# Performance work log

Hardware: AMD Instinct MI355X
Metric: run time of the kernel (lower is better)

The kernel has to match this reference:

```python
import jax, jax.numpy as jnp
import numpy as np

N_NODES = 100000
N_EDGES = 1600000
IN_CH = 1024
FEAT_CH = 128
OUT_CH = 3


def setup_inputs() -> dict:
    key = jax.random.key(0)
    ks = jax.random.split(key, 9)
    features = jax.random.normal(ks[0], (N_NODES, IN_CH), dtype=jnp.float32)
    edges = jax.random.randint(ks[1], (2, N_EDGES), 0, N_NODES, dtype=jnp.int64)
    edges2 = jax.random.randint(ks[2], (2, N_EDGES), 0, N_NODES, dtype=jnp.int64)
    edge_features = jax.random.normal(ks[3], (N_EDGES, 1), dtype=jnp.float32)
    additional_feature = jax.random.normal(ks[4], (N_NODES, 20), dtype=jnp.float32)
    # GCNConv linear weights (glorot-ish scale) and biases
    W1 = jax.random.normal(ks[5], (IN_CH, FEAT_CH), dtype=jnp.float32) * (1.0 / np.sqrt(IN_CH))
    b1 = jnp.zeros((FEAT_CH,), dtype=jnp.float32)
    W2 = jax.random.normal(ks[6], (FEAT_CH, OUT_CH), dtype=jnp.float32) * (1.0 / np.sqrt(FEAT_CH))
    b2 = jnp.zeros((OUT_CH,), dtype=jnp.float32)
    return {"features": features, "edges": edges, "edges2": edges2,
            "edge_features": edge_features, "additional_feature": additional_feature,
            "W1": W1, "b1": b1, "W2": W2, "b2": b2}


def gcn_conv(x, edge_index, W, b, num_nodes):
    """PyG GCNConv: x' = D^{-1/2}(A+I)D^{-1/2} x W + b (self-loops added)."""
    x = x @ W  # project first (cheaper feature dim for aggregation)
    loop = jnp.arange(num_nodes, dtype=edge_index.dtype)
    src = jnp.concatenate([edge_index[0], loop])
    dst = jnp.concatenate([edge_index[1], loop])
    deg = jax.ops.segment_sum(jnp.ones_like(dst, dtype=x.dtype), dst,
                              num_segments=num_nodes)  # >=1 due to self-loops
    dinv = jax.lax.rsqrt(deg)
    norm = dinv[src] * dinv[dst]  # [E+N]
    out = jax.ops.segment_sum(x[src] * norm[:, None], dst, num_segments=num_nodes)
    return out + b


def reference(features, edges, edges2, edge_features, additional_feature, W1, b1, W2, b2):
    # use_additional_channels=False -> features unchanged; edge_features forced to None
    n = features.shape[0]
    x = gcn_conv(features, edges2, W1, b1, n)
    x = jax.nn.relu(x)
    # dropout inactive in eval mode
    return gcn_conv(x, edges2, W2, b2, n)
```

## Files before the change

kernel.cpp:

```cpp
#include <hip/hip_runtime.h>
#include <hip/hip_bf16.h>

typedef __attribute__((ext_vector_type(8))) _Float16 half8;
typedef __attribute__((ext_vector_type(4))) float f32x4;

#define N_NODES 100000
#define N_EDGES 1600000
#define IN_CH 1024
#define FEAT 128
#define CAP 64
#define NDIG 196
#define CAPC 10240
#define NGB ((N_NODES + 127) / 128)

__device__ __forceinline__ void gload16(const void* g, void* l) {
    __builtin_amdgcn_global_load_lds(
        (const __attribute__((address_space(1))) unsigned int*)g,
        (__attribute__((address_space(3))) unsigned int*)l, 16, 0, 0);
}

__global__ void k_prep(const float* __restrict__ W1, _Float16* __restrict__ Bf,
                       int* __restrict__ cursorC, int* __restrict__ done) {
    int idx = blockIdx.x * 256 + threadIdx.x;
    if (idx < IN_CH * FEAT) {
        int col = idx & (FEAT - 1), k = idx >> 7;
        int cf = col >> 4, s = k >> 5;
        int lane = ((k >> 3) & 3) * 16 + (col & 15);
        int e = k & 7;
        Bf[(((cf * 32 + s) * 64 + lane) << 3) + e] = (_Float16)W1[idx];
    }
    if (idx < NDIG) cursorC[idx] = idx * CAPC;
    if (idx == 0) *done = 0;
}

__global__ __launch_bounds__(256, 2) void k_build_gemm(
    const float* __restrict__ A, const _Float16* __restrict__ Bf,
    const int4* __restrict__ src4, const int4* __restrict__ dst4,
    int* __restrict__ cursorC, uint2* __restrict__ recs,
    int* __restrict__ csr, int* __restrict__ cnt, float* __restrict__ dinvarr,
    int* __restrict__ done, _Float16* __restrict__ H, int M, int e4)
{
    __shared__ union {
        float As[2][8192];
        struct { int hist[NDIG], segoff[NDIG], lcur[NDIG]; } bin;
        int cl[512];
    } sm;
    const int t = threadIdx.x;

    if (blockIdx.x < NDIG) {
        const int b = blockIdx.x;
        if (t < NDIG) sm.bin.hist[t] = 0;
        __syncthreads();
        const int base4 = b * 2048;
        int4 sv[8], dv[8];
#pragma unroll
        for (int j = 0; j < 8; ++j) {
            int idx = base4 + j * 256 + t;
            if (idx < e4) { sv[j] = src4[idx]; dv[j] = dst4[idx]; }
            else { sv[j] = (int4){-1,-1,-1,-1}; dv[j] = (int4){-1,-1,-1,-1}; }
        }
#pragma unroll
        for (int j = 0; j < 8; ++j) {
            int dd[4] = {dv[j].x, dv[j].y, dv[j].z, dv[j].w};
            int ss[4] = {sv[j].x, sv[j].y, sv[j].z, sv[j].w};
#pragma unroll
            for (int c = 0; c < 4; ++c)
                if ((unsigned)dd[c] < N_NODES && (unsigned)ss[c] < N_NODES)
                    atomicAdd(&sm.bin.hist[dd[c] >> 9], 1);
        }
        __syncthreads();
        if (t < NDIG) {
            sm.bin.segoff[t] = atomicAdd(&cursorC[t], sm.bin.hist[t]);
            sm.bin.lcur[t] = 0;
        }
        __syncthreads();
#pragma unroll
        for (int j = 0; j < 8; ++j) {
            int dd[4] = {dv[j].x, dv[j].y, dv[j].z, dv[j].w};
            int ss[4] = {sv[j].x, sv[j].y, sv[j].z, sv[j].w};
#pragma unroll
            for (int c = 0; c < 4; ++c) {
                if ((unsigned)dd[c] < N_NODES && (unsigned)ss[c] < N_NODES) {
                    int dg = dd[c] >> 9;
                    int r = atomicAdd(&sm.bin.lcur[dg], 1);
                    int pos = sm.bin.segoff[dg] + r;
                    if (pos < (dg + 1) * CAPC)
                        recs[pos] = (uint2){(unsigned)ss[c], (unsigned)dd[c]};
                }
            }
        }
        __syncthreads();
        if (t == 0) {
            __threadfence();
            __hip_atomic_fetch_add(done, 1, __ATOMIC_RELEASE, __HIP_MEMORY_SCOPE_AGENT);
            while (__hip_atomic_load(done, __ATOMIC_ACQUIRE, __HIP_MEMORY_SCOPE_AGENT) < NDIG)
                __builtin_amdgcn_s_sleep(8);
        }
        __syncthreads();
        const int d = blockIdx.x;
        for (int j = t; j < 512; j += 256) sm.cl[j] = 0;
        __syncthreads();
        const int base = d * CAPC;
        int n = cursorC[d] - base;
        if (n > CAPC) n = CAPC;
        for (int k = t; k < n; k += 256) {
            uint2 r = recs[base + k];
            int local = (int)r.y & 511;
            int slot = atomicAdd(&sm.cl[local], 1);
            if (slot < CAP) csr[((int)r.y << 6) + slot] = (int)r.x;
        }
        __syncthreads();
        const int node0 = d << 9;
        for (int j = t; j < 512; j += 256) {
            int node = node0 + j;
            if (node < N_NODES) {
                int c = sm.cl[j] < CAP ? sm.cl[j] : CAP;
                cnt[node] = c;
                dinvarr[node] = rsqrtf((float)(c + 1));
            }
        }
        return;
    }

    const int gb = blockIdx.x - NDIG;
    const int brow0 = gb << 7;
    const int wid = t >> 6, lane = t & 63;

    const char* gsrc[8];
#pragma unroll
    for (int i = 0; i < 8; ++i) {
        int R = (wid * 8 + i) * 4 + (lane >> 4);
        int grow = brow0 + R; if (grow >= M) grow = M - 1;
        int gcol = ((lane & 15) * 16) ^ ((R & 15) << 4);
        gsrc[i] = (const char*)A + (size_t)grow * 4096 + gcol;
    }

#define STAGE(buf, kt)                                                          \
    {                                                                           \
        _Pragma("unroll") for (int i = 0; i < 8; ++i)                           \
            gload16(gsrc[i] + (kt) * 256,                                       \
                    (char*)sm.As[buf] + (wid * 8 + i) * 1024);                  \
    }
#define LOADB(dst, s)                                                           \
    {                                                                           \
        _Pragma("unroll") for (int cf = 0; cf < 8; ++cf)                        \
            dst[cf] = *(const half8*)(Bf + (((cf * 32 + (s)) << 9)) + lane * 8);\
    }
#define AFRAG(dst, cur, rf, kk)                                                 \
    {                                                                           \
        int R_ = wid * 32 + (rf) * 16 + (lane & 15);                            \
        int k0_ = (kk) * 128 + (lane >> 4) * 32;                                \
        int sw_ = (R_ & 15) << 4;                                               \
        f32x4 lo_ = *(const f32x4*)((char*)sm.As[cur] + R_ * 256 + (k0_ ^ sw_));\
        f32x4 hi_ = *(const f32x4*)((char*)sm.As[cur] + R_ * 256 + ((k0_ + 16) ^ sw_)); \
        dst[0] = (_Float16)lo_.x; dst[1] = (_Float16)lo_.y;                     \
        dst[2] = (_Float16)lo_.z; dst[3] = (_Float16)lo_.w;                     \
        dst[4] = (_Float16)hi_.x; dst[5] = (_Float16)hi_.y;                     \
        dst[6] = (_Float16)hi_.z; dst[7] = (_Float16)hi_.w;                     \
    }

    f32x4 acc[2][8];
#pragma unroll
    for (int rf = 0; rf < 2; ++rf)
#pragma unroll
        for (int cf = 0; cf < 8; ++cf) acc[rf][cf] = (f32x4){0.f, 0.f, 0.f, 0.f};

    half8 bbA[8], bbB[8];
    STAGE(0, 0);
    LOADB(bbA, 0);
    __syncthreads();

    int cur = 0;
#pragma unroll 1
    for (int kt = 0; kt < 16; ++kt) {
        if (kt < 15) STAGE(cur ^ 1, kt + 1);
        const int s = kt * 2;
        LOADB(bbB, s + 1);
        {
            half8 a0, a1;
            AFRAG(a0, cur, 0, 0);
            AFRAG(a1, cur, 1, 0);
#pragma unroll
            for (int cf = 0; cf < 8; ++cf) {
                acc[0][cf] = __builtin_amdgcn_mfma_f32_16x16x32_f16(a0, bbA[cf], acc[0][cf], 0, 0, 0);
                acc[1][cf] = __builtin_amdgcn_mfma_f32_16x16x32_f16(a1, bbA[cf], acc[1][cf], 0, 0, 0);
            }
        }
        if (s + 2 < 32) LOADB(bbA, s + 2);
        {
            half8 a0, a1;
            AFRAG(a0, cur, 0, 1);
            AFRAG(a1, cur, 1, 1);
#pragma unroll
            for (int cf = 0; cf < 8; ++cf) {
                acc[0][cf] = __builtin_amdgcn_mfma_f32_16x16x32_f16(a0, bbB[cf], acc[0][cf], 0, 0, 0);
                acc[1][cf] = __builtin_amdgcn_mfma_f32_16x16x32_f16(a1, bbB[cf], acc[1][cf], 0, 0, 0);
            }
        }
        __syncthreads();
        cur ^= 1;
    }
#undef STAGE
#undef LOADB
#undef AFRAG

    {
        int colb = lane & 15, rgrp = (lane >> 4) * 4;
#pragma unroll
        for (int rf = 0; rf < 2; ++rf) {
#pragma unroll
            for (int r = 0; r < 4; ++r) {
                int grow = brow0 + wid * 32 + rf * 16 + rgrp + r;
                if (grow < M) {
                    _Float16* hp = H + (size_t)grow * FEAT + colb;
#pragma unroll
                    for (int cf = 0; cf < 8; ++cf)
                        hp[cf * 16] = (_Float16)acc[rf][cf][r];
                }
            }
        }
    }
}

__global__ __launch_bounds__(256) void k_agg1(const _Float16* __restrict__ H,
                                              const int* __restrict__ csr,
                                              const int* __restrict__ cnt,
                                              const float* __restrict__ dinvarr,
                                              const float* __restrict__ b1,
                                              const float* __restrict__ W2,
                                              float* __restrict__ Y, int n) {
    int wid = threadIdx.x >> 6, lane = threadIdx.x & 63;
    int i = blockIdx.x * 4 + wid;
    if (i >= n) return;
    const int g = lane >> 4, u = lane & 15;
    int m = cnt[i];
    float di = dinvarr[i];

    int sl; float dl;
    if (lane < m) { sl = csr[(i << 6) + lane]; dl = dinvarr[sl]; }
    else          { sl = i;                    dl = (lane == m) ? di : 0.f; }
    int mm = (m < 63 ? m : 63) + 1;

    float ax[8];
#pragma unroll
    for (int j = 0; j < 8; ++j) ax[j] = 0.f;

    for (int e = 0; e < mm; e += 16) {
        int idx0 = e + g, idx1 = e + 4 + g, idx2 = e + 8 + g, idx3 = e + 12 + g;
        bool v0 = idx0 < mm, v1 = idx1 < mm, v2 = idx2 < mm, v3 = idx3 < mm;
        int c0i = v0 ? idx0 : 0, c1i = v1 ? idx1 : 0;
        int c2i = v2 ? idx2 : 0, c3i = v3 ? idx3 : 0;
        int s0 = __shfl(sl, c0i); float w0 = __shfl(dl, c0i);
        int s1 = __shfl(sl, c1i); float w1 = __shfl(dl, c1i);
        int s2 = __shfl(sl, c2i); float w2 = __shfl(dl, c2i);
        int s3 = __shfl(sl, c3i); float w3 = __shfl(dl, c3i);
        if (!v0) { s0 = i; w0 = 0.f; }
        if (!v1) { s1 = i; w1 = 0.f; }
        if (!v2) { s2 = i; w2 = 0.f; }
        if (!v3) { s3 = i; w3 = 0.f; }
        half8 h0 = *(const half8*)(H + ((size_t)s0 << 7) + u * 8);
        half8 h1 = *(const half8*)(H + ((size_t)s1 << 7) + u * 8);
        half8 h2 = *(const half8*)(H + ((size_t)s2 << 7) + u * 8);
        half8 h3 = *(const half8*)(H + ((size_t)s3 << 7) + u * 8);
#pragma unroll
        for (int j = 0; j < 8; ++j)
            ax[j] += w0 * (float)h0[j] + w1 * (float)h1[j]
                   + w2 * (float)h2[j] + w3 * (float)h3[j];
    }

#pragma unroll
    for (int j = 0; j < 8; ++j) {
        ax[j] += __shfl_xor(ax[j], 16);
        ax[j] += __shfl_xor(ax[j], 32);
    }

    int c0 = u * 8;
    float y0 = 0.f, y1 = 0.f, y2 = 0.f;
#pragma unroll
    for (int j = 0; j < 8; ++j) {
        float x = di * ax[j] + b1[c0 + j];
        x = x > 0.f ? x : 0.f;
        y0 += x * W2[(c0 + j) * 3 + 0];
        y1 += x * W2[(c0 + j) * 3 + 1];
        y2 += x * W2[(c0 + j) * 3 + 2];
    }
#pragma unroll
    for (int d = 1; d < 16; d <<= 1) {
        y0 += __shfl_xor(y0, d);
        y1 += __shfl_xor(y1, d);
        y2 += __shfl_xor(y2, d);
    }
    if (lane == 0) {
        float* yp = Y + (size_t)i * 4;
        yp[0] = di * y0; yp[1] = di * y1; yp[2] = di * y2;
    }
}

__global__ void k_agg2(const float* __restrict__ Y, const int* __restrict__ csr,
                       const int* __restrict__ cnt, const float* __restrict__ dinvarr,
                       const float* __restrict__ b2, float* __restrict__ out, int n) {
    int i = blockIdx.x * 256 + threadIdx.x;
    if (i >= n) return;
    int m = cnt[i];
    float di = dinvarr[i];
    int base = i << 6;
    const float4* Y4 = (const float4*)Y;
    float4 self = Y4[i];
    float a0 = self.x, a1 = self.y, a2 = self.z;
    int e = 0;
    for (; e + 3 < m; e += 4) {
        int s0 = csr[base + e],     s1 = csr[base + e + 1];
        int s2 = csr[base + e + 2], s3 = csr[base + e + 3];
        float4 v0 = Y4[s0], v1 = Y4[s1], v2 = Y4[s2], v3 = Y4[s3];
        a0 += (v0.x + v1.x) + (v2.x + v3.x);
        a1 += (v0.y + v1.y) + (v2.y + v3.y);
        a2 += (v0.z + v1.z) + (v2.z + v3.z);
    }
    for (; e < m; ++e) {
        float4 v0 = Y4[csr[base + e]];
        a0 += v0.x; a1 += v0.y; a2 += v0.z;
    }
    out[(size_t)i * 3 + 0] = di * a0 + b2[0];
    out[(size_t)i * 3 + 1] = di * a1 + b2[1];
    out[(size_t)i * 3 + 2] = di * a2 + b2[2];
}

extern "C" void kernel_launch(void* const* d_in, const int* in_sizes, int n_in,
                              void* d_out, int out_size, void* d_ws, size_t ws_size,
                              hipStream_t stream) {
    const float* features = (const float*)d_in[0];
    const int* edges2 = (const int*)d_in[2];
    const float* W1 = (const float*)d_in[5];
    const float* b1 = (const float*)d_in[6];
    const float* W2 = (const float*)d_in[7];
    const float* b2 = (const float*)d_in[8];
    float* out = (float*)d_out;

    const int N = N_NODES, E = N_EDGES;
    const int4* src4 = (const int4*)edges2;
    const int4* dst4 = (const int4*)(edges2 + E);
    int e4 = E / 4;

    char* p = (char*)d_ws;
    auto carve = [&](size_t bytes) { char* q = p; p += (bytes + 255) & ~(size_t)255; return q; };
    int* cnt       = (int*)carve(4 * (size_t)N);
    float* dinvarr = (float*)carve(4 * (size_t)N);
    int* cursorC   = (int*)carve(4 * NDIG);
    int* done      = (int*)carve(4);
    uint2* recs    = (uint2*)carve(8 * (size_t)NDIG * CAPC);
    int* csr       = (int*)carve(4 * (size_t)N * CAP);
    _Float16* Bf   = (_Float16*)carve(2 * (size_t)IN_CH * FEAT);
    _Float16* H    = (_Float16*)carve(2 * (size_t)N * FEAT);
    float* Y       = (float*)carve(16 * (size_t)N);

    k_prep<<<dim3(512), dim3(256), 0, stream>>>(W1, Bf, cursorC, done);
    k_build_gemm<<<dim3(NDIG + NGB), dim3(256), 0, stream>>>(
        features, Bf, src4, dst4, cursorC, recs, csr, cnt, dinvarr, done, H, N, e4);
    k_agg1<<<dim3((N + 3) / 4), dim3(256), 0, stream>>>(H, csr, cnt, dinvarr, b1, W2, Y, N);
    k_agg2<<<dim3((N + 255) / 256), dim3(256), 0, stream>>>(Y, csr, cnt, dinvarr, b2, out, N);
}
```

Before: 244.6 us.

## Make GEMM A staging warp-private with 4-deep pipeline and vmcnt waits

Each wave now stages only its own 32 rows of A into a private LDS region, with a 4-slot ring of 32-wide k-slices. Completion is tracked with explicit s_waitcnt vmcnt counts instead of block-wide __syncthreads. This removes block barriers from the GEMM main loop and deepens prefetch to hide global-load latency. The risk is that the hand-computed vmcnt values must match the exact number of outstanding loads per wave, including the B-fragment loads, or results will be wrong.

```diff
diff --git a/kernel.cpp b/kernel.cpp
--- a/kernel.cpp
+++ b/kernel.cpp
@@ -18,6 +18,12 @@
         (const __attribute__((address_space(1))) unsigned int*)g,
         (__attribute__((address_space(3))) unsigned int*)l, 16, 0, 0);
 }
+
+#define WAITV(n)                                                               \
+    do {                                                                       \
+        asm volatile("s_waitcnt vmcnt(" #n ")" ::: "memory");                  \
+        __builtin_amdgcn_sched_barrier(0);                                     \
+    } while (0)
 
 __global__ void k_prep(const float* __restrict__ W1, _Float16* __restrict__ Bf,
                        int* __restrict__ cursorC, int* __restrict__ done) {
@@ -41,7 +47,7 @@
     int* __restrict__ done, _Float16* __restrict__ H, int M, int e4)
 {
     __shared__ union {
-        float As[2][8192];
+        float As[16384];
         struct { int hist[NDIG], segoff[NDIG], lcur[NDIG]; } bin;
         int cl[512];
     } sm;
@@ -125,38 +131,46 @@
     const int gb = blockIdx.x - NDIG;
     const int brow0 = gb << 7;
     const int wid = t >> 6, lane = t & 63;
-
-    const char* gsrc[8];
-#pragma unroll
-    for (int i = 0; i < 8; ++i) {
-        int R = (wid * 8 + i) * 4 + (lane >> 4);
-        int grow = brow0 + R; if (grow >= M) grow = M - 1;
-        int gcol = ((lane & 15) * 16) ^ ((R & 15) << 4);
+    char* ldsw = (char*)sm.As + wid * 16384;
+
+    const char* gsrc[4];
+#pragma unroll
+    for (int i = 0; i < 4; ++i) {
+        int grow = brow0 + wid * 32 + i * 8 + (lane >> 3);
+        if (grow >= M) grow = M - 1;
+        int gcol = ((lane & 7) * 16) ^ ((lane >> 3) << 4);
         gsrc[i] = (const char*)A + (size_t)grow * 4096 + gcol;
     }
-
-#define STAGE(buf, kt)                                                          \
+    const _Float16* pbw = Bf + lane * 8;
+
+#define STAGE(bi, ks)                                                           \
     {                                                                           \
-        _Pragma("unroll") for (int i = 0; i < 8; ++i)                           \
-            gload16(gsrc[i] + (kt) * 256,                                       \
-                    (char*)sm.As[buf] + (wid * 8 + i) * 1024);                  \
-    }
-#define LOADB(dst, s)                                                           \
+        _Pragma("unroll") for (int i = 0; i < 4; ++i)                           \
+            gload16(gsrc[i] + (ks) * 128, ldsw + (bi) * 4096 + i * 1024);       \
+    }
+#define LOADB8(dst, ks)                                                         \
     {                                                                           \
         _Pragma("unroll") for (int cf = 0; cf < 8; ++cf)                        \
-            dst[cf] = *(const half8*)(Bf + (((cf * 32 + (s)) << 9)) + lane * 8);\
-    }
-#define AFRAG(dst, cur, rf, kk)                                                 \
+            dst[cf] = *(const half8*)(pbw + ((size_t)((cf * 32 + (ks)) << 9))); \
+    }
+#define MFMA_STEP(bi, bset)                                                     \
     {                                                                           \
-        int R_ = wid * 32 + (rf) * 16 + (lane & 15);                            \
-        int k0_ = (kk) * 128 + (lane >> 4) * 32;                                \
-        int sw_ = (R_ & 15) << 4;                                               \
-        f32x4 lo_ = *(const f32x4*)((char*)sm.As[cur] + R_ * 256 + (k0_ ^ sw_));\
-        f32x4 hi_ = *(const f32x4*)((char*)sm.As[cur] + R_ * 256 + ((k0_ + 16) ^ sw_)); \
-        dst[0] = (_Float16)lo_.x; dst[1] = (_Float16)lo_.y;                     \
-        dst[2] = (_Float16)lo_.z; dst[3] = (_Float16)lo_.w;                     \
-        dst[4] = (_Float16)hi_.x; dst[5] = (_Float16)hi_.y;                     \
-        dst[6] = (_Float16)hi_.z; dst[7] = (_Float16)hi_.w;                     \
+        const char* base_ = ldsw + (bi) * 4096;                                 \
+        _Pragma("unroll") for (int rf = 0; rf < 2; ++rf) {                      \
+            int lr_ = rf * 16 + (lane & 15);                                    \
+            int k0_ = (lane >> 4) * 32;                                         \
+            int sw_ = (lr_ & 7) << 4;                                           \
+            f32x4 lo_ = *(const f32x4*)(base_ + lr_ * 128 + (k0_ ^ sw_));       \
+            f32x4 hi_ = *(const f32x4*)(base_ + lr_ * 128 + ((k0_ + 16) ^ sw_));\
+            half8 a_;                                                           \
+            a_[0] = (_Float16)lo_.x; a_[1] = (_Float16)lo_.y;                   \
+            a_[2] = (_Float16)lo_.z; a_[3] = (_Float16)lo_.w;                   \
+            a_[4] = (_Float16)hi_.x; a_[5] = (_Float16)hi_.y;                   \
+            a_[6] = (_Float16)hi_.z; a_[7] = (_Float16)hi_.w;                   \
+            _Pragma("unroll") for (int cf = 0; cf < 8; ++cf)                    \
+                acc[rf][cf] = __builtin_amdgcn_mfma_f32_16x16x32_f16(           \
+                    a_, bset[cf], acc[rf][cf], 0, 0, 0);                        \
+        }                                                                       \
     }
 
     f32x4 acc[2][8];
@@ -165,44 +179,29 @@
 #pragma unroll
         for (int cf = 0; cf < 8; ++cf) acc[rf][cf] = (f32x4){0.f, 0.f, 0.f, 0.f};
 
-    half8 bbA[8], bbB[8];
-    STAGE(0, 0);
-    LOADB(bbA, 0);
-    __syncthreads();
-
-    int cur = 0;
+    half8 bA[8], bB[8];
+
+    STAGE(0, 0); STAGE(1, 1); STAGE(2, 2);
+    LOADB8(bA, 0);
+
 #pragma unroll 1
-    for (int kt = 0; kt < 16; ++kt) {
-        if (kt < 15) STAGE(cur ^ 1, kt + 1);
-        const int s = kt * 2;
-        LOADB(bbB, s + 1);
-        {
-            half8 a0, a1;
-            AFRAG(a0, cur, 0, 0);
-            AFRAG(a1, cur, 1, 0);
-#pragma unroll
-            for (int cf = 0; cf < 8; ++cf) {
-                acc[0][cf] = __builtin_amdgcn_mfma_f32_16x16x32_f16(a0, bbA[cf], acc[0][cf], 0, 0, 0);
-                acc[1][cf] = __builtin_amdgcn_mfma_f32_16x16x32_f16(a1, bbA[cf], acc[1][cf], 0, 0, 0);
-            }
-        }
-        if (s + 2 < 32) LOADB(bbA, s + 2);
-        {
-            half8 a0, a1;
-            AFRAG(a0, cur, 0, 1);
-            AFRAG(a1, cur, 1, 1);
-#pragma unroll
-            for (int cf = 0; cf < 8; ++cf) {
-                acc[0][cf] = __builtin_amdgcn_mfma_f32_16x16x32_f16(a0, bbB[cf], acc[0][cf], 0, 0, 0);
-                acc[1][cf] = __builtin_amdgcn_mfma_f32_16x16x32_f16(a1, bbB[cf], acc[1][cf], 0, 0, 0);
-            }
-        }
-        __syncthreads();
-        cur ^= 1;
+    for (int kt = 0; kt < 32; kt += 2) {
+        LOADB8(bB, kt + 1);
+        if (kt + 3 < 32) STAGE((kt + 3) & 3, kt + 3);
+        if (kt == 0)       WAITV(12);
+        else if (kt == 30) WAITV(8);
+        else               WAITV(16);
+        MFMA_STEP(kt & 3, bA);
+        if (kt + 2 < 32) LOADB8(bA, kt + 2);
+        if (kt + 4 < 32) STAGE((kt + 4) & 3, kt + 4);
+        if (kt == 28)      WAITV(12);
+        else if (kt == 30) WAITV(0);
+        else               WAITV(16);
+        MFMA_STEP((kt + 1) & 3, bB);
     }
 #undef STAGE
-#undef LOADB
-#undef AFRAG
+#undef LOADB8
+#undef MFMA_STEP
 
     {
         int colb = lane & 15, rgrp = (lane >> 4) * 4;
```

Result: slower. 266.3 us (+8.9%).
